# Kernel optimization log

Hardware: AMD Instinct MI355X
Metric: run time of the kernel (lower is better)

Reference implementation:

```python
import jax, jax.numpy as jnp
import numpy as np

N = 100000          # number of active sparse points
GRID = 800          # coordinate grid extent (2D)
KS = 9              # 3x3 kernel offsets
C_IN = 24
C_HID = 144         # round(24 * 6)
C_OUT = 24
EPS = 1e-5


def _build_kernel_map():
    """Build MinkowskiEngine-style kernel map for a 3x3 stride-1 channelwise conv.
    Returns (in_idx, out_idx, off_id), each [KS*N] int32. Invalid (no neighbor)
    entries point to sentinel row N so the padded gather/scatter is a no-op."""
    rng = np.random.default_rng(0)
    flat = rng.choice(GRID * GRID, size=N, replace=False)  # unique 2D coords
    ys, xs = flat // GRID, flat % GRID
    coord_to_idx = -np.ones(GRID * GRID, dtype=np.int64)
    coord_to_idx[flat] = np.arange(N)
    in_chunks, out_chunks, off_chunks = [], [], []
    pts = np.arange(N, dtype=np.int64)
    k = 0
    for dy in (-1, 0, 1):
        for dx in (-1, 0, 1):
            ny, nx = ys + dy, xs + dx
            inside = (ny >= 0) & (ny < GRID) & (nx >= 0) & (nx < GRID)
            nflat = np.clip(ny, 0, GRID - 1) * GRID + np.clip(nx, 0, GRID - 1)
            nidx = np.where(inside, coord_to_idx[nflat], -1)
            valid = nidx >= 0
            in_chunks.append(np.where(valid, nidx, N))
            out_chunks.append(np.where(valid, pts, N))
            off_chunks.append(np.full(N, k, dtype=np.int64))
            k += 1
    in_idx = np.concatenate(in_chunks).astype(np.int32)
    out_idx = np.concatenate(out_chunks).astype(np.int32)
    off_id = np.concatenate(off_chunks).astype(np.int32)
    return in_idx, out_idx, off_id


def setup_inputs() -> dict:
    key = jax.random.key(0)
    ks = jax.random.split(key, 4)
    in_idx, out_idx, off_id = _build_kernel_map()
    return {
        "feats": jax.random.normal(ks[0], (N, C_IN), jnp.float32),
        "w1": jax.random.normal(ks[1], (C_IN, C_HID), jnp.float32) * 0.1,
        "g1": jnp.ones((C_HID,), jnp.float32),
        "b1": jnp.zeros((C_HID,), jnp.float32),
        "w2": jax.random.normal(ks[2], (KS, C_HID), jnp.float32) * 0.1,
        "g2": jnp.ones((C_HID,), jnp.float32),
        "b2": jnp.zeros((C_HID,), jnp.float32),
        "w3": jax.random.normal(ks[3], (C_HID, C_OUT), jnp.float32) * 0.1,
        "g3": jnp.ones((C_OUT,), jnp.float32),
        "b3": jnp.zeros((C_OUT,), jnp.float32),
        "in_idx": jnp.asarray(in_idx),
        "out_idx": jnp.asarray(out_idx),
        "off_id": jnp.asarray(off_id),
    }


def _bn(x, g, b):
    # MinkowskiBatchNorm forward (training mode): per-channel stats over points
    m = jnp.mean(x, axis=0)
    v = jnp.var(x, axis=0)
    return (x - m) * jax.lax.rsqrt(v + EPS) * g + b


def _relu6(x):
    return jnp.clip(x, 0.0, 6.0)


def _channelwise_conv3x3(x, w2, in_idx, out_idx, off_id):
    # gather-multiply-scatter: out[p, c] = sum_k w2[k, c] * x[nbr_k(p), c]
    xp = jnp.concatenate([x, jnp.zeros((1, x.shape[1]), x.dtype)], axis=0)  # sentinel row
    contrib = xp[in_idx] * w2[off_id]                     # [KS*N, C_HID]
    out = jnp.zeros((N + 1, x.shape[1]), x.dtype).at[out_idx].add(contrib)
    return out[:N]


def reference(feats, w1, g1, b1, w2, g2, b2, w3, g3, b3, in_idx, out_idx, off_id):
    x = _relu6(_bn(feats @ w1, g1, b1))                   # 1x1 expand
    x = _relu6(_bn(_channelwise_conv3x3(x, w2, in_idx, out_idx, off_id), g2, b2))
    x = _bn(x @ w3, g3, b3)                               # 1x1 project
    return x + feats                                      # residual (in==out, stride==1)
```

## Files before the change

### kernel.cpp

```cpp
#include <hip/hip_runtime.h>
#include <hip/hip_fp16.h>

#define N_PTS 100000
#define KSZ 9
#define C_IN 24
#define C_HID 144
#define C_OUT 24
#define G4_HID 36
#define G8_HID 18
#define G4_OUT 6
#define EPSV 1e-5f

#define X1H_B     0
#define X2H_B     28800288
#define Y3F_O     14400072
#define ST_O      16800072
#define MU1_O     (ST_O + 0)
#define M1_O      (ST_O + 32)
#define SC1_O     (ST_O + 640)
#define SH1_O     (ST_O + 800)
#define SUM2_O    (ST_O + 960)
#define SQ2_O     (ST_O + 1120)
#define SC2_O     (ST_O + 1280)
#define SH2_O     (ST_O + 1440)
#define SUM3_O    (ST_O + 1600)
#define SQ3_O     (ST_O + 1632)
#define SC3_O     (ST_O + 1664)
#define SH3_O     (ST_O + 1696)
#define ST_SIZE   1728

__device__ inline float4 f4z() { return make_float4(0.f, 0.f, 0.f, 0.f); }
__device__ inline float4 f4_add(float4 a, float4 b) {
    return make_float4(a.x + b.x, a.y + b.y, a.z + b.z, a.w + b.w);
}
__device__ inline float4 f4_fma4(float4 a, float4 b, float4 c) {
    return make_float4(fmaf(a.x, b.x, c.x), fmaf(a.y, b.y, c.y),
                       fmaf(a.z, b.z, c.z), fmaf(a.w, b.w, c.w));
}
__device__ inline float4 f4_fma_s(float s, float4 b, float4 c) {
    return make_float4(fmaf(s, b.x, c.x), fmaf(s, b.y, c.y),
                       fmaf(s, b.z, c.z), fmaf(s, b.w, c.w));
}
__device__ inline float4 f4_clamp6(float4 a) {
    return make_float4(fminf(fmaxf(a.x, 0.f), 6.f), fminf(fmaxf(a.y, 0.f), 6.f),
                       fminf(fmaxf(a.z, 0.f), 6.f), fminf(fmaxf(a.w, 0.f), 6.f));
}
__device__ inline unsigned pack2(float a, float b) {
    __half2 h = __floats2half2_rn(a, b);
    return *reinterpret_cast<unsigned*>(&h);
}
__device__ inline float2 uph(unsigned u) {
    __half2 h = *reinterpret_cast<__half2*>(&u);
    return __half22float2(h);
}

__global__ __launch_bounds__(256) void k_init(float* ws) {
    int t = threadIdx.x;
    for (int i = t; i < ST_SIZE; i += 256) ws[ST_O + i] = 0.f;
    if (t < G8_HID) {
        uint4 z; z.x = 0u; z.y = 0u; z.z = 0u; z.w = 0u;
        ((uint4*)ws)[(size_t)N_PTS * G8_HID + t] = z;
    }
}

#define MROWS 128
__device__ inline float task_acc(const float* tile, int cnt, int task) {
    if (task < 576) {
        int i = task / 24, j = task % 24;
        float a = 0.f;
        for (int r = 0; r < cnt; r++) a += tile[r * 24 + i] * tile[r * 24 + j];
        return a;
    }
    int k = task - 576;
    float a = 0.f;
    for (int r = 0; r < cnt; r++) a += tile[r * 24 + k];
    return a;
}
__global__ __launch_bounds__(256) void k_moments(const float* __restrict__ feats,
                                                 float* __restrict__ ws) {
    __shared__ float tile[MROWS * C_IN];
    int t = threadIdx.x;
    float acc0 = 0.f, acc1 = 0.f, acc2 = 0.f;
    int nChunks = (N_PTS + MROWS - 1) / MROWS;
    for (int ch = blockIdx.x; ch < nChunks; ch += gridDim.x) {
        int r0 = ch * MROWS;
        int cnt = min(MROWS, N_PTS - r0);
        __syncthreads();
        for (int e = t; e < cnt * C_IN; e += 256) tile[e] = feats[(size_t)r0 * C_IN + e];
        __syncthreads();
        acc0 += task_acc(tile, cnt, t);
        acc1 += task_acc(tile, cnt, t + 256);
        if (t < 88) acc2 += task_acc(tile, cnt, t + 512);
    }
    atomicAdd(&ws[M1_O + t], acc0);
    atomicAdd(&ws[M1_O + t + 256], acc1);
    if (t < 88) {
        int task = t + 512;
        if (task < 576) atomicAdd(&ws[M1_O + task], acc2);
        else            atomicAdd(&ws[MU1_O + task - 576], acc2);
    }
}

__global__ void k_fin1(const float* __restrict__ w1, const float* __restrict__ g1,
                       const float* __restrict__ b1, float* __restrict__ ws) {
    int c = threadIdx.x;
    if (c >= C_HID) return;
    float wc[C_IN];
    for (int k = 0; k < C_IN; k++) wc[k] = w1[k * C_HID + c];
    const float invN = 1.f / (float)N_PTS;
    float mean = 0.f;
    for (int k = 0; k < C_IN; k++) mean += ws[MU1_O + k] * wc[k];
    mean *= invN;
    float e2 = 0.f;
    for (int i = 0; i < C_IN; i++) {
        float s = 0.f;
        for (int j = 0; j < C_IN; j++) s += ws[M1_O + i * 24 + j] * wc[j];
        e2 += wc[i] * s;
    }
    e2 *= invN;
    float var = e2 - mean * mean;
    float s1 = g1[c] * rsqrtf(var + EPSV);
    ws[SC1_O + c] = s1;
    ws[SH1_O + c] = b1[c] - mean * s1;
}

__global__ __launch_bounds__(256) void k_gemm1(const float* __restrict__ feats,
                                               const float* __restrict__ w1,
                                               float* __restrict__ ws) {
    __shared__ float4 w1s[C_IN * G4_HID];
    __shared__ float4 sc[G4_HID], sh[G4_HID];
    int t = threadIdx.x;
    for (int e = t; e < C_IN * G4_HID; e += 256) w1s[e] = ((const float4*)w1)[e];
    if (t < G4_HID) {
        sc[t] = ((const float4*)(ws + SC1_O))[t];
        sh[t] = ((const float4*)(ws + SH1_O))[t];
    }
    __syncthreads();
    uint4* x1u = (uint4*)ws;
    const int T = N_PTS * G8_HID;
    for (int tau = blockIdx.x * 256 + t; tau < T; tau += gridDim.x * 256) {
        int p = tau / G8_HID;
        int g = tau % G8_HID;
        const float4* fr = (const float4*)(feats + (size_t)p * C_IN);
        float4 a0 = f4z(), a1 = f4z();
#pragma unroll
        for (int q = 0; q < 6; q++) {
            float4 fq = fr[q];
            a0 = f4_fma_s(fq.x, w1s[(4 * q + 0) * G4_HID + 2 * g], a0);
            a1 = f4_fma_s(fq.x, w1s[(4 * q + 0) * G4_HID + 2 * g + 1], a1);
            a0 = f4_fma_s(fq.y, w1s[(4 * q + 1) * G4_HID + 2 * g], a0);
            a1 = f4_fma_s(fq.y, w1s[(4 * q + 1) * G4_HID + 2 * g + 1], a1);
            a0 = f4_fma_s(fq.z, w1s[(4 * q + 2) * G4_HID + 2 * g], a0);
            a1 = f4_fma_s(fq.z, w1s[(4 * q + 2) * G4_HID + 2 * g + 1], a1);
            a0 = f4_fma_s(fq.w, w1s[(4 * q + 3) * G4_HID + 2 * g], a0);
            a1 = f4_fma_s(fq.w, w1s[(4 * q + 3) * G4_HID + 2 * g + 1], a1);
        }
        a0 = f4_clamp6(f4_fma4(a0, sc[2 * g], sh[2 * g]));
        a1 = f4_clamp6(f4_fma4(a1, sc[2 * g + 1], sh[2 * g + 1]));
        uint4 o;
        o.x = pack2(a0.x, a0.y); o.y = pack2(a0.z, a0.w);
        o.z = pack2(a1.x, a1.y); o.w = pack2(a1.z, a1.w);
        x1u[tau] = o;
    }
}

__global__ __launch_bounds__(256) void k_conv(const float* __restrict__ w2,
                                              const int* __restrict__ in_idx,
                                              float* __restrict__ ws) {
    __shared__ float lsum[C_HID], lsq[C_HID];
    int t = threadIdx.x;
    if (t < C_HID) { lsum[t] = 0.f; lsq[t] = 0.f; }
    __syncthreads();
    const uint4* x1u = (const uint4*)ws;
    uint4* x2u = (uint4*)((char*)ws + X2H_B);
    bool active = t < 252;
    int pt = t / G8_HID, g = t % G8_HID;
    const float4* w2v = (const float4*)w2;
    float4 wA[KSZ], wB[KSZ];
#pragma unroll
    for (int k = 0; k < KSZ; k++) {
        wA[k] = w2v[k * G4_HID + 2 * g];
        wB[k] = w2v[k * G4_HID + 2 * g + 1];
    }
    float4 rsA = f4z(), rsB = f4z(), rqA = f4z(), rqB = f4z();
    int nChunks = (N_PTS + 13) / 14;
    for (int ch = blockIdx.x; ch < nChunks; ch += gridDim.x) {
        int p = ch * 14 + pt;
        if (active && p < N_PTS) {
            int idx[KSZ];
#pragma unroll
            for (int k = 0; k < KSZ; k++) idx[k] = in_idx[k * N_PTS + p];
            float4 aA = f4z(), aB = f4z();
#pragma unroll
            for (int k = 0; k < KSZ; k++) {
                uint4 v = x1u[(size_t)idx[k] * G8_HID + g];
                float2 f0 = uph(v.x), f1 = uph(v.y), f2 = uph(v.z), f3 = uph(v.w);
                aA = f4_fma4(wA[k], make_float4(f0.x, f0.y, f1.x, f1.y), aA);
                aB = f4_fma4(wB[k], make_float4(f2.x, f2.y, f3.x, f3.y), aB);
            }
            uint4 o;
            o.x = pack2(aA.x, aA.y); o.y = pack2(aA.z, aA.w);
            o.z = pack2(aB.x, aB.y); o.w = pack2(aB.z, aB.w);
            x2u[(size_t)p * G8_HID + g] = o;
            rsA = f4_add(rsA, aA); rsB = f4_add(rsB, aB);
            rqA = f4_fma4(aA, aA, rqA); rqB = f4_fma4(aB, aB, rqB);
        }
    }
    if (active) {
        int c0 = 8 * g;
        atomicAdd(&lsum[c0 + 0], rsA.x); atomicAdd(&lsum[c0 + 1], rsA.y);
        atomicAdd(&lsum[c0 + 2], rsA.z); atomicAdd(&lsum[c0 + 3], rsA.w);
        atomicAdd(&lsum[c0 + 4], rsB.x); atomicAdd(&lsum[c0 + 5], rsB.y);
        atomicAdd(&lsum[c0 + 6], rsB.z); atomicAdd(&lsum[c0 + 7], rsB.w);
        atomicAdd(&lsq[c0 + 0], rqA.x);  atomicAdd(&lsq[c0 + 1], rqA.y);
        atomicAdd(&lsq[c0 + 2], rqA.z);  atomicAdd(&lsq[c0 + 3], rqA.w);
        atomicAdd(&lsq[c0 + 4], rqB.x);  atomicAdd(&lsq[c0 + 5], rqB.y);
        atomicAdd(&lsq[c0 + 6], rqB.z);  atomicAdd(&lsq[c0 + 7], rqB.w);
    }
    __syncthreads();
    if (t < C_HID) {
        atomicAdd(&ws[SUM2_O + t], lsum[t]);
        atomicAdd(&ws[SQ2_O + t], lsq[t]);
    }
}

__global__ void k_fin2(const float* __restrict__ g2, const float* __restrict__ b2,
                       float* __restrict__ ws) {
    int c = threadIdx.x;
    if (c >= C_HID) return;
    const float invN = 1.f / (float)N_PTS;
    float mean = ws[SUM2_O + c] * invN;
    float var = ws[SQ2_O + c] * invN - mean * mean;
    float s = g2[c] * rsqrtf(var + EPSV);
    ws[SC2_O + c] = s;
    ws[SH2_O + c] = b2[c] - mean * s;
}

#define TP 64
__global__ __launch_bounds__(256) void k_gemm2(const float* __restrict__ w3,
                                               float* __restrict__ ws) {
    __shared__ float xs[TP * 145];
    __shared__ float w3s[C_HID * C_OUT];
    __shared__ float sc2s[C_HID], sh2s[C_HID];
    __shared__ float ssum[C_OUT], ssq[C_OUT];
    int t = threadIdx.x;
    for (int e = t; e < C_HID * C_OUT / 4; e += 256)
        ((float4*)w3s)[e] = ((const float4*)w3)[e];
    if (t < C_HID) { sc2s[t] = ws[SC2_O + t]; sh2s[t] = ws[SH2_O + t]; }
    if (t < C_OUT) { ssum[t] = 0.f; ssq[t] = 0.f; }
    __syncthreads();
    const uint4* x2u = (const uint4*)((char*)ws + X2H_B);
    int p0 = blockIdx.x * TP;
    for (int e = t; e < TP * G8_HID; e += 256) {
        int row = e / G8_HID, col = e % G8_HID;
        int p = p0 + row;
        int c0 = 8 * col;
        float v[8];
        if (p < N_PTS) {
            uint4 u = x2u[(size_t)p * G8_HID + col];
            float2 f0 = uph(u.x), f1 = uph(u.y), f2 = uph(u.z), f3 = uph(u.w);
            v[0] = f0.x; v[1] = f0.y; v[2] = f1.x; v[3] = f1.y;
            v[4] = f2.x; v[5] = f2.y; v[6] = f3.x; v[7] = f3.y;
#pragma unroll
            for (int i = 0; i < 8; i++)
                v[i] = fminf(fmaxf(fmaf(v[i], sc2s[c0 + i], sh2s[c0 + i]), 0.f), 6.f);
        } else {
#pragma unroll
            for (int i = 0; i < 8; i++) v[i] = 0.f;
        }
#pragma unroll
        for (int i = 0; i < 8; i++) xs[row * 145 + c0 + i] = v[i];
    }
    __syncthreads();
    int pl = t & 63, cg = t >> 6;
    int c0 = 6 * cg;
    float acc[6] = {0.f, 0.f, 0.f, 0.f, 0.f, 0.f};
    const float* xr = xs + pl * 145;
#pragma unroll 4
    for (int h = 0; h < C_HID; h++) {
        float x = xr[h];
#pragma unroll
        for (int j = 0; j < 6; j++) acc[j] = fmaf(x, w3s[h * C_OUT + c0 + j], acc[j]);
    }
    int p = p0 + pl;
    bool valid = p < N_PTS;
    float* y3 = ws + Y3F_O;
    if (valid) {
#pragma unroll
        for (int j = 0; j < 6; j++) y3[(size_t)p * C_OUT + c0 + j] = acc[j];
    }
    float s[6], q[6];
#pragma unroll
    for (int j = 0; j < 6; j++) {
        s[j] = valid ? acc[j] : 0.f;
        q[j] = s[j] * s[j];
    }
#pragma unroll
    for (int off = 32; off > 0; off >>= 1) {
#pragma unroll
        for (int j = 0; j < 6; j++) {
            s[j] += __shfl_down(s[j], off);
            q[j] += __shfl_down(q[j], off);
        }
    }
    if (pl == 0) {
#pragma unroll
        for (int j = 0; j < 6; j++) {
            atomicAdd(&ssum[c0 + j], s[j]);
            atomicAdd(&ssq[c0 + j], q[j]);
        }
    }
    __syncthreads();
    if (t < C_OUT) {
        atomicAdd(&ws[SUM3_O + t], ssum[t]);
        atomicAdd(&ws[SQ3_O + t], ssq[t]);
    }
}

__global__ void k_fin3(const float* __restrict__ g3, const float* __restrict__ b3,
                       float* __restrict__ ws) {
    int c = threadIdx.x;
    if (c >= C_OUT) return;
    const float invN = 1.f / (float)N_PTS;
    float mean = ws[SUM3_O + c] * invN;
    float var = ws[SQ3_O + c] * invN - mean * mean;
    float s = g3[c] * rsqrtf(var + EPSV);
    ws[SC3_O + c] = s;
    ws[SH3_O + c] = b3[c] - mean * s;
}

__global__ __launch_bounds__(256) void k_out(const float* __restrict__ feats,
                                             const float* __restrict__ ws,
                                             float* __restrict__ out) {
    int t4 = blockIdx.x * 256 + threadIdx.x;
    const int T = N_PTS * G4_OUT;
    if (t4 >= T) return;
    int g = t4 % G4_OUT;
    float4 y = ((const float4*)(ws + Y3F_O))[t4];
    float4 s = ((const float4*)(ws + SC3_O))[g];
    float4 b = ((const float4*)(ws + SH3_O))[g];
    float4 f = ((const float4*)feats)[t4];
    ((float4*)out)[t4] = f4_add(f4_fma4(y, s, b), f);
}

extern "C" void kernel_launch(void* const* d_in, const int* in_sizes, int n_in,
                              void* d_out, int out_size, void* d_ws, size_t ws_size,
                              hipStream_t stream) {
    const float* feats = (const float*)d_in[0];
    const float* w1 = (const float*)d_in[1];
    const float* g1 = (const float*)d_in[2];
    const float* b1 = (const float*)d_in[3];
    const float* w2 = (const float*)d_in[4];
    const float* g2 = (const float*)d_in[5];
    const float* b2 = (const float*)d_in[6];
    const float* w3 = (const float*)d_in[7];
    const float* g3 = (const float*)d_in[8];
    const float* b3 = (const float*)d_in[9];
    const int* in_idx = (const int*)d_in[10];
    float* ws = (float*)d_ws;
    float* out = (float*)d_out;

    hipLaunchKernelGGL(k_init, dim3(1), dim3(256), 0, stream, ws);
    hipLaunchKernelGGL(k_moments, dim3(256), dim3(256), 0, stream, feats, ws);
    hipLaunchKernelGGL(k_fin1, dim3(1), dim3(192), 0, stream, w1, g1, b1, ws);
    hipLaunchKernelGGL(k_gemm1, dim3(2048), dim3(256), 0, stream, feats, w1, ws);
    hipLaunchKernelGGL(k_conv, dim3(2048), dim3(256), 0, stream, w2, in_idx, ws);
    hipLaunchKernelGGL(k_fin2, dim3(1), dim3(192), 0, stream, g2, b2, ws);
    hipLaunchKernelGGL(k_gemm2, dim3((N_PTS + TP - 1) / TP), dim3(256), 0, stream, w3, ws);
    hipLaunchKernelGGL(k_fin3, dim3(1), dim3(64), 0, stream, g3, b3, ws);
    hipLaunchKernelGGL(k_out, dim3((N_PTS * G4_OUT + 255) / 256), dim3(256), 0, stream,
                       feats, ws, out);
}
```

Measured before the change: 319.9 us.

## Fold BN finalize kernels into consumers and replace init kernel with memsets

Removes the three single-block BN finalize kernels and the init kernel. Each consumer kernel (gemm1, gemm2, out) now recomputes its per-channel scale and shift in shared memory at block start, and the workspace zeroing becomes two async memsets. This cuts launch count and the serial tiny-kernel gaps at the cost of redundant per-block stats math. The conv kernel now reads w2 from shared memory instead of registers and gets a 6-blocks occupancy hint, and gemm1's grid shrinks from 2048 to 512 blocks to amortise its heavier per-block prologue.

```diff
diff --git a/kernel.cpp b/kernel.cpp
--- a/kernel.cpp
+++ b/kernel.cpp
@@ -11,23 +11,17 @@
 #define G4_OUT 6
 #define EPSV 1e-5f
 
-#define X1H_B     0
 #define X2H_B     28800288
+#define SENT_B    28800000
 #define Y3F_O     14400072
 #define ST_O      16800072
+#define ST_B      67200288
 #define MU1_O     (ST_O + 0)
 #define M1_O      (ST_O + 32)
-#define SC1_O     (ST_O + 640)
-#define SH1_O     (ST_O + 800)
-#define SUM2_O    (ST_O + 960)
-#define SQ2_O     (ST_O + 1120)
-#define SC2_O     (ST_O + 1280)
-#define SH2_O     (ST_O + 1440)
-#define SUM3_O    (ST_O + 1600)
-#define SQ3_O     (ST_O + 1632)
-#define SC3_O     (ST_O + 1664)
-#define SH3_O     (ST_O + 1696)
-#define ST_SIZE   1728
+#define SUM2_O    (ST_O + 640)
+#define SQ2_O     (ST_O + 800)
+#define SUM3_O    (ST_O + 960)
+#define SQ3_O     (ST_O + 992)
 
 __device__ inline float4 f4z() { return make_float4(0.f, 0.f, 0.f, 0.f); }
 __device__ inline float4 f4_add(float4 a, float4 b) {
@@ -52,15 +46,6 @@
 __device__ inline float2 uph(unsigned u) {
     __half2 h = *reinterpret_cast<__half2*>(&u);
     return __half22float2(h);
-}
-
-__global__ __launch_bounds__(256) void k_init(float* ws) {
-    int t = threadIdx.x;
-    for (int i = t; i < ST_SIZE; i += 256) ws[ST_O + i] = 0.f;
-    if (t < G8_HID) {
-        uint4 z; z.x = 0u; z.y = 0u; z.z = 0u; z.w = 0u;
-        ((uint4*)ws)[(size_t)N_PTS * G8_HID + t] = z;
-    }
 }
 
 #define MROWS 128
@@ -101,41 +86,46 @@
     }
 }
 
-__global__ void k_fin1(const float* __restrict__ w1, const float* __restrict__ g1,
-                       const float* __restrict__ b1, float* __restrict__ ws) {
-    int c = threadIdx.x;
-    if (c >= C_HID) return;
-    float wc[C_IN];
-    for (int k = 0; k < C_IN; k++) wc[k] = w1[k * C_HID + c];
-    const float invN = 1.f / (float)N_PTS;
-    float mean = 0.f;
-    for (int k = 0; k < C_IN; k++) mean += ws[MU1_O + k] * wc[k];
-    mean *= invN;
-    float e2 = 0.f;
-    for (int i = 0; i < C_IN; i++) {
-        float s = 0.f;
-        for (int j = 0; j < C_IN; j++) s += ws[M1_O + i * 24 + j] * wc[j];
-        e2 += wc[i] * s;
-    }
-    e2 *= invN;
-    float var = e2 - mean * mean;
-    float s1 = g1[c] * rsqrtf(var + EPSV);
-    ws[SC1_O + c] = s1;
-    ws[SH1_O + c] = b1[c] - mean * s1;
-}
-
 __global__ __launch_bounds__(256) void k_gemm1(const float* __restrict__ feats,
                                                const float* __restrict__ w1,
+                                               const float* __restrict__ g1,
+                                               const float* __restrict__ b1,
                                                float* __restrict__ ws) {
     __shared__ float4 w1s[C_IN * G4_HID];
-    __shared__ float4 sc[G4_HID], sh[G4_HID];
+    __shared__ float M1s[576];
+    __shared__ float MU1s[24];
+    __shared__ float scf[C_HID], shf[C_HID];
     int t = threadIdx.x;
     for (int e = t; e < C_IN * G4_HID; e += 256) w1s[e] = ((const float4*)w1)[e];
-    if (t < G4_HID) {
-        sc[t] = ((const float4*)(ws + SC1_O))[t];
-        sh[t] = ((const float4*)(ws + SH1_O))[t];
-    }
-    __syncthreads();
+    for (int e = t; e < 576; e += 256) M1s[e] = ws[M1_O + e];
+    if (t < 24) MU1s[t] = ws[MU1_O + t];
+    __syncthreads();
+    if (t < C_HID) {
+        const float* w1f = (const float*)w1s;
+        float wc[C_IN];
+#pragma unroll
+        for (int k = 0; k < C_IN; k++) wc[k] = w1f[k * C_HID + t];
+        const float invN = 1.f / (float)N_PTS;
+        float mean = 0.f;
+#pragma unroll
+        for (int k = 0; k < C_IN; k++) mean += MU1s[k] * wc[k];
+        mean *= invN;
+        float e2 = 0.f;
+        for (int i = 0; i < C_IN; i++) {
+            float s = 0.f;
+#pragma unroll
+            for (int j = 0; j < C_IN; j++) s += M1s[i * 24 + j] * wc[j];
+            e2 += wc[i] * s;
+        }
+        e2 *= invN;
+        float var = e2 - mean * mean;
+        float s1 = g1[t] * rsqrtf(var + EPSV);
+        scf[t] = s1;
+        shf[t] = b1[t] - mean * s1;
+    }
+    __syncthreads();
+    const float4* sc4 = (const float4*)scf;
+    const float4* sh4 = (const float4*)shf;
     uint4* x1u = (uint4*)ws;
     const int T = N_PTS * G8_HID;
     for (int tau = blockIdx.x * 256 + t; tau < T; tau += gridDim.x * 256) {
@@ -155,8 +145,8 @@
             a0 = f4_fma_s(fq.w, w1s[(4 * q + 3) * G4_HID + 2 * g], a0);
             a1 = f4_fma_s(fq.w, w1s[(4 * q + 3) * G4_HID + 2 * g + 1], a1);
         }
-        a0 = f4_clamp6(f4_fma4(a0, sc[2 * g], sh[2 * g]));
-        a1 = f4_clamp6(f4_fma4(a1, sc[2 * g + 1], sh[2 * g + 1]));
+        a0 = f4_clamp6(f4_fma4(a0, sc4[2 * g], sh4[2 * g]));
+        a1 = f4_clamp6(f4_fma4(a1, sc4[2 * g + 1], sh4[2 * g + 1]));
         uint4 o;
         o.x = pack2(a0.x, a0.y); o.y = pack2(a0.z, a0.w);
         o.z = pack2(a1.x, a1.y); o.w = pack2(a1.z, a1.w);
@@ -164,24 +154,19 @@
     }
 }
 
-__global__ __launch_bounds__(256) void k_conv(const float* __restrict__ w2,
-                                              const int* __restrict__ in_idx,
-                                              float* __restrict__ ws) {
+__global__ __launch_bounds__(256, 6) void k_conv(const float* __restrict__ w2,
+                                                 const int* __restrict__ in_idx,
+                                                 float* __restrict__ ws) {
+    __shared__ float4 w2s[KSZ * G4_HID];
     __shared__ float lsum[C_HID], lsq[C_HID];
     int t = threadIdx.x;
+    for (int e = t; e < KSZ * G4_HID; e += 256) w2s[e] = ((const float4*)w2)[e];
     if (t < C_HID) { lsum[t] = 0.f; lsq[t] = 0.f; }
     __syncthreads();
     const uint4* x1u = (const uint4*)ws;
     uint4* x2u = (uint4*)((char*)ws + X2H_B);
     bool active = t < 252;
     int pt = t / G8_HID, g = t % G8_HID;
-    const float4* w2v = (const float4*)w2;
-    float4 wA[KSZ], wB[KSZ];
-#pragma unroll
-    for (int k = 0; k < KSZ; k++) {
-        wA[k] = w2v[k * G4_HID + 2 * g];
-        wB[k] = w2v[k * G4_HID + 2 * g + 1];
-    }
     float4 rsA = f4z(), rsB = f4z(), rqA = f4z(), rqB = f4z();
     int nChunks = (N_PTS + 13) / 14;
     for (int ch = blockIdx.x; ch < nChunks; ch += gridDim.x) {
@@ -195,8 +180,8 @@
             for (int k = 0; k < KSZ; k++) {
                 uint4 v = x1u[(size_t)idx[k] * G8_HID + g];
                 float2 f0 = uph(v.x), f1 = uph(v.y), f2 = uph(v.z), f3 = uph(v.w);
-                aA = f4_fma4(wA[k], make_float4(f0.x, f0.y, f1.x, f1.y), aA);
-                aB = f4_fma4(wB[k], make_float4(f2.x, f2.y, f3.x, f3.y), aB);
+                aA = f4_fma4(w2s[k * G4_HID + 2 * g], make_float4(f0.x, f0.y, f1.x, f1.y), aA);
+                aB = f4_fma4(w2s[k * G4_HID + 2 * g + 1], make_float4(f2.x, f2.y, f3.x, f3.y), aB);
             }
             uint4 o;
             o.x = pack2(aA.x, aA.y); o.y = pack2(aA.z, aA.w);
@@ -224,20 +209,10 @@
     }
 }
 
-__global__ void k_fin2(const float* __restrict__ g2, const float* __restrict__ b2,
-                       float* __restrict__ ws) {
-    int c = threadIdx.x;
-    if (c >= C_HID) return;
-    const float invN = 1.f / (float)N_PTS;
-    float mean = ws[SUM2_O + c] * invN;
-    float var = ws[SQ2_O + c] * invN - mean * mean;
-    float s = g2[c] * rsqrtf(var + EPSV);
-    ws[SC2_O + c] = s;
-    ws[SH2_O + c] = b2[c] - mean * s;
-}
-
 #define TP 64
 __global__ __launch_bounds__(256) void k_gemm2(const float* __restrict__ w3,
+                                               const float* __restrict__ g2,
+                                               const float* __restrict__ b2,
                                                float* __restrict__ ws) {
     __shared__ float xs[TP * 145];
     __shared__ float w3s[C_HID * C_OUT];
@@ -246,7 +221,14 @@
     int t = threadIdx.x;
     for (int e = t; e < C_HID * C_OUT / 4; e += 256)
         ((float4*)w3s)[e] = ((const float4*)w3)[e];
-    if (t < C_HID) { sc2s[t] = ws[SC2_O + t]; sh2s[t] = ws[SH2_O + t]; }
+    if (t < C_HID) {
+        const float invN = 1.f / (float)N_PTS;
+        float mean = ws[SUM2_O + t] * invN;
+        float var = ws[SQ2_O + t] * invN - mean * mean;
+        float s = g2[t] * rsqrtf(var + EPSV);
+        sc2s[t] = s;
+        sh2s[t] = b2[t] - mean * s;
+    }
     if (t < C_OUT) { ssum[t] = 0.f; ssq[t] = 0.f; }
     __syncthreads();
     const uint4* x2u = (const uint4*)((char*)ws + X2H_B);
@@ -317,28 +299,29 @@
     }
 }
 
-__global__ void k_fin3(const float* __restrict__ g3, const float* __restrict__ b3,
-                       float* __restrict__ ws) {
-    int c = threadIdx.x;
-    if (c >= C_OUT) return;
-    const float invN = 1.f / (float)N_PTS;
-    float mean = ws[SUM3_O + c] * invN;
-    float var = ws[SQ3_O + c] * invN - mean * mean;
-    float s = g3[c] * rsqrtf(var + EPSV);
-    ws[SC3_O + c] = s;
-    ws[SH3_O + c] = b3[c] - mean * s;
-}
-
 __global__ __launch_bounds__(256) void k_out(const float* __restrict__ feats,
+                                             const float* __restrict__ g3,
+                                             const float* __restrict__ b3,
                                              const float* __restrict__ ws,
                                              float* __restrict__ out) {
-    int t4 = blockIdx.x * 256 + threadIdx.x;
+    __shared__ float scs[C_OUT], shs[C_OUT];
+    int t = threadIdx.x;
+    if (t < C_OUT) {
+        const float invN = 1.f / (float)N_PTS;
+        float mean = ws[SUM3_O + t] * invN;
+        float var = ws[SQ3_O + t] * invN - mean * mean;
+        float s = g3[t] * rsqrtf(var + EPSV);
+        scs[t] = s;
+        shs[t] = b3[t] - mean * s;
+    }
+    __syncthreads();
+    int t4 = blockIdx.x * 256 + t;
     const int T = N_PTS * G4_OUT;
     if (t4 >= T) return;
     int g = t4 % G4_OUT;
     float4 y = ((const float4*)(ws + Y3F_O))[t4];
-    float4 s = ((const float4*)(ws + SC3_O))[g];
-    float4 b = ((const float4*)(ws + SH3_O))[g];
+    float4 s = ((const float4*)scs)[g];
+    float4 b = ((const float4*)shs)[g];
     float4 f = ((const float4*)feats)[t4];
     ((float4*)out)[t4] = f4_add(f4_fma4(y, s, b), f);
 }
@@ -360,14 +343,14 @@
     float* ws = (float*)d_ws;
     float* out = (float*)d_out;
 
-    hipLaunchKernelGGL(k_init, dim3(1), dim3(256), 0, stream, ws);
+    hipMemsetAsync((char*)d_ws + ST_B, 0, 4096, stream);
+    hipMemsetAsync((char*)d_ws + SENT_B, 0, 288, stream);
+
     hipLaunchKernelGGL(k_moments, dim3(256), dim3(256), 0, stream, feats, ws);
-    hipLaunchKernelGGL(k_fin1, dim3(1), dim3(192), 0, stream, w1, g1, b1, ws);
-    hipLaunchKernelGGL(k_gemm1, dim3(2048), dim3(256), 0, stream, feats, w1, ws);
+    hipLaunchKernelGGL(k_gemm1, dim3(512), dim3(256), 0, stream, feats, w1, g1, b1, ws);
     hipLaunchKernelGGL(k_conv, dim3(2048), dim3(256), 0, stream, w2, in_idx, ws);
-    hipLaunchKernelGGL(k_fin2, dim3(1), dim3(192), 0, stream, g2, b2, ws);
-    hipLaunchKernelGGL(k_gemm2, dim3((N_PTS + TP - 1) / TP), dim3(256), 0, stream, w3, ws);
-    hipLaunchKernelGGL(k_fin3, dim3(1), dim3(64), 0, stream, g3, b3, ws);
+    hipLaunchKernelGGL(k_gemm2, dim3((N_PTS + TP - 1) / TP), dim3(256), 0, stream,
+                       w3, g2, b2, ws);
     hipLaunchKernelGGL(k_out, dim3((N_PTS * G4_OUT + 255) / 256), dim3(256), 0, stream,
-                       feats, ws, out);
-}
+                       feats, g3, b3, ws, out);
+}
```

Result: faster. 312.9 us (-2.2%).
